# Optimization experiments

Hardware: AMD Instinct MI355X
Metric: run time of the kernel (lower is better)

Reference implementation:

```python
import jax, jax.numpy as jnp
import numpy as np

K = 10  # topk classes


def setup_inputs() -> dict:
    key = jax.random.key(0)
    ks = jax.random.split(key, 12)
    B, DF, M, C, V, DW, DT = 64, 768, 26, 3129, 10000, 300, 1024
    s = lambda k, sh, scale: jax.random.normal(k, sh, dtype=jnp.float32) * scale
    return {
        "ftm": s(ks[0], (B, DF, M, M), 1.0),
        "logits": s(ks[1], (B, C), 1.0),
        "labels": jax.random.randint(ks[2], (B,), 0, C, dtype=jnp.int32),
        "indices_table": jax.random.randint(ks[3], (C, 4), 0, V, dtype=jnp.int32),
        "word2vec": s(ks[4], (V, DW), 1.0),
        "W_emb": s(ks[5], (DW, DT), 1.0 / np.sqrt(DW)),
        "b_emb": jnp.zeros((DT,), jnp.float32),
        "W_cls": s(ks[6], (DT, DT), 1.0 / np.sqrt(DT)),
        "b_cls": jnp.zeros((DT,), jnp.float32),
        "W_v": s(ks[7], (DF, DT), 1.0 / np.sqrt(DF)),
        "b_v": jnp.zeros((DT,), jnp.float32),
        "W_bap": s(ks[8], (DT, DT), 1.0 / np.sqrt(DT)),
        "b_bap": jnp.zeros((DT,), jnp.float32),
        "W_fc": s(ks[9], (DT, K), 1.0 / np.sqrt(DT)),
        "b_fc": jnp.zeros((K,), jnp.float32),
    }


def reference(ftm, logits, labels, indices_table, word2vec,
              W_emb, b_emb, W_cls, b_cls, W_v, b_v, W_bap, b_bap, W_fc, b_fc):
    B, DF = ftm.shape[0], ftm.shape[1]
    C = logits.shape[1]
    # dispatch: topk classes, gather their word indices, embed
    _, topk_idx = jax.lax.top_k(logits, K)                  # [B, K]
    topk_cls = indices_table[topk_idx]                      # [B, K, 4]
    emb = word2vec[topk_cls].mean(axis=2)                   # [B, K, 300] (ClassEmbedding pooling)
    cls_emb = jax.nn.relu(emb @ W_emb + b_emb)              # [B, K, 1024]
    # SAC_BAP (dropouts in eval mode = identity)
    cls_emb = jax.nn.relu(cls_emb @ W_cls + b_cls)          # [B, K, 1024]
    f = ftm.reshape(B, DF, -1).transpose(0, 2, 1)           # [B, F, 768], F = m*m
    v = jax.nn.relu(f @ W_v + b_v)                          # [B, F, 1024]
    att_w_b_sfx = jnp.einsum('bfd,bkd->bfk', v, cls_emb)    # [B, F, K]
    att_w = jax.nn.softmax(att_w_b_sfx, axis=1)             # softmax over positions
    bap = jnp.einsum('bfd,bfk,bkd->bd', v, att_w, cls_emb)  # [B, 1024]
    bap = jax.nn.relu(bap @ W_bap + b_bap)                  # bap_emb_FC
    bap_logits = bap @ W_fc + b_fc                          # fc_new 1x1 conv -> [B, K]
    # combine: scatter topk logits into the full class space
    um = jnp.zeros((B, C), dtype=bap_logits.dtype)
    um = um.at[jnp.arange(B)[:, None], topk_idx].set(bap_logits)
    return um
```

## Files before the change

kernel.cpp:

```cpp
#include <hip/hip_runtime.h>
#include <hip/hip_bf16.h>

#define B_   64
#define C_   3129
#define K_   10
#define DF_  768
#define F_   676
#define DW_  300
#define DWP_ 320
#define DT_  1024
#define NSEG 13
#define FSEG 52

typedef __attribute__((ext_vector_type(8))) short short8;
typedef __attribute__((ext_vector_type(4))) float floatx4;

__device__ __forceinline__ void gload_lds16(const void* g, void* l) {
    __builtin_amdgcn_global_load_lds(
        (const __attribute__((address_space(1))) void*)g,
        (__attribute__((address_space(3))) void*)l, 16, 0, 0);
}

__global__ void topk_kernel(const float* __restrict__ logits,
                            int* __restrict__ topk_idx) {
    __shared__ float vals[C_];
    __shared__ float red_v[256];
    __shared__ int   red_i[256];
    int b = blockIdx.x;
    int tid = threadIdx.x;
    for (int i = tid; i < C_; i += 256) vals[i] = logits[(size_t)b * C_ + i];
    __syncthreads();
    for (int sel = 0; sel < K_; ++sel) {
        float bv = -INFINITY; int bi = 0x7fffffff;
        for (int i = tid; i < C_; i += 256) {
            float v = vals[i];
            if (v > bv) { bv = v; bi = i; }
        }
        red_v[tid] = bv; red_i[tid] = bi;
        __syncthreads();
        for (int s = 128; s > 0; s >>= 1) {
            if (tid < s) {
                float ov = red_v[tid + s]; int oi = red_i[tid + s];
                if (ov > red_v[tid] || (ov == red_v[tid] && oi < red_i[tid])) {
                    red_v[tid] = ov; red_i[tid] = oi;
                }
            }
            __syncthreads();
        }
        if (tid == 0) {
            topk_idx[b * K_ + sel] = red_i[0];
            vals[red_i[0]] = -INFINITY;
        }
        __syncthreads();
    }
}

__global__ void emb_kernel(const int* __restrict__ topk_idx,
                           const int* __restrict__ indices_table,
                           const float* __restrict__ word2vec,
                           __hip_bfloat16* __restrict__ emb) {
    int idx = blockIdx.x * blockDim.x + threadIdx.x;
    if (idx >= B_ * K_ * DWP_) return;
    int j  = idx % DWP_;
    int bk = idx / DWP_;
    float s = 0.f;
    if (j < DW_) {
        int cls = topk_idx[bk];
        const int* tbl = indices_table + (size_t)cls * 4;
        #pragma unroll
        for (int i = 0; i < 4; ++i) s += word2vec[(size_t)tbl[i] * DW_ + j];
        s *= 0.25f;
    }
    emb[idx] = (__hip_bfloat16)s;
}

__device__ __forceinline__ void tp_body(const float* __restrict__ s,
                                        __hip_bfloat16* __restrict__ d,
                                        int R, int Cc, int Rp, int c0, int r0) {
    __shared__ float tile[64][65];
    int t = threadIdx.x;
    int cl = (t & 15) * 4;
    int rl = t >> 4;
    #pragma unroll
    for (int i = 0; i < 4; ++i) {
        int r = rl + i * 16;
        float4 v = make_float4(0.f, 0.f, 0.f, 0.f);
        if (r0 + r < R && c0 + cl < Cc)
            v = *(const float4*)(s + (size_t)(r0 + r) * Cc + c0 + cl);
        tile[r][cl + 0] = v.x; tile[r][cl + 1] = v.y;
        tile[r][cl + 2] = v.z; tile[r][cl + 3] = v.w;
    }
    __syncthreads();
    int cw = t >> 2;
    int r4 = (t & 3) * 16;
    if (c0 + cw < Cc) {
        __align__(16) __hip_bfloat16 buf[16];
        #pragma unroll
        for (int j = 0; j < 16; ++j) buf[j] = (__hip_bfloat16)tile[r4 + j][cw];
        float4* dp = (float4*)(d + (size_t)(c0 + cw) * Rp + r0 + r4);
        dp[0] = *(float4*)&buf[0];
        dp[1] = *(float4*)&buf[8];
    }
}

__global__ __launch_bounds__(256)
void transpose_ftm(const float* __restrict__ src, __hip_bfloat16* __restrict__ dst) {
    tp_body(src + (size_t)blockIdx.z * DF_ * F_,
            dst + (size_t)blockIdx.z * F_ * DF_,
            DF_, F_, DF_, blockIdx.x * 64, blockIdx.y * 64);
}

__global__ __launch_bounds__(256)
void transpose_weights(const float* __restrict__ Wemb, __hip_bfloat16* __restrict__ WembT,
                       const float* __restrict__ Wcls, __hip_bfloat16* __restrict__ WclsT,
                       const float* __restrict__ Wv,   __hip_bfloat16* __restrict__ WvT,
                       const float* __restrict__ Wbap, __hip_bfloat16* __restrict__ WbapT) {
    int id = blockIdx.x;
    const float* s; __hip_bfloat16* d; int R, Rp;
    if (id < 80)       { s = Wemb; d = WembT; R = DW_;  Rp = DWP_; }
    else if (id < 336) { s = Wcls; d = WclsT; R = DT_;  Rp = DT_;  id -= 80;  }
    else if (id < 528) { s = Wv;   d = WvT;   R = DF_;  Rp = DF_;  id -= 336; }
    else               { s = Wbap; d = WbapT; R = DT_;  Rp = DT_;  id -= 528; }
    int bx = id & 15;
    int by = id >> 4;
    tp_body(s, d, R, DT_, Rp, bx * 64, by * 64);
}

template <int RELU, int OUTBF>
__global__ __launch_bounds__(256)
void gemm_mfma(const __hip_bfloat16* __restrict__ A,
               const __hip_bfloat16* __restrict__ Bt,
               const float* __restrict__ bias,
               void* __restrict__ Cout, int M, int N, int Kp) {
    __shared__ __align__(16) char smem[34816];
    __hip_bfloat16* As = (__hip_bfloat16*)smem;
    __hip_bfloat16* Bs = As + 128 * 64;
    int tid = threadIdx.x;
    int wave = tid >> 6, lane = tid & 63;
    int quad = lane >> 4, l16 = lane & 15;
    int wm = (wave & 1) * 64, wn = (wave >> 1) * 64;

    int gx = gridDim.x;
    int nwg = gx * gridDim.y;
    int flat = blockIdx.y * gx + blockIdx.x;
    int q = nwg >> 3, r = nwg & 7;
    int xcd = flat & 7, lid = flat >> 3;
    int o = (xcd < r ? xcd * (q + 1) : r * (q + 1) + (xcd - r) * q) + lid;
    int n0 = (o % gx) * 128;
    int m0 = (o / gx) * 128;

    floatx4 acc[4][4];
    #pragma unroll
    for (int i = 0; i < 4; ++i)
        #pragma unroll
        for (int j = 0; j < 4; ++j)
            acc[i][j] = (floatx4){0.f, 0.f, 0.f, 0.f};

    int rsub = lane >> 3;
    int gchunk = (lane & 7) ^ rsub;

    int arow[4], brow[4];
    #pragma unroll
    for (int i = 0; i < 4; ++i) {
        arow[i] = wm + i * 16 + l16;
        brow[i] = wn + i * 16 + l16;
    }

    for (int k0 = 0; k0 < Kp; k0 += 64) {
        #pragma unroll
        for (int c = 0; c < 4; ++c) {
            int grp = wave * 4 + c;
            int row = grp * 8 + rsub;
            int ra = m0 + row; if (ra >= M) ra = M - 1;
            gload_lds16(A + (size_t)ra * Kp + k0 + gchunk * 8, As + grp * 512);
            gload_lds16(Bt + (size_t)(n0 + row) * Kp + k0 + gchunk * 8, Bs + grp * 512);
        }
        __syncthreads();
        #pragma unroll
        for (int ks = 0; ks < 2; ++ks) {
            short8 af[4], bf[4];
            #pragma unroll
            for (int mi = 0; mi < 4; ++mi)
                af[mi] = *(const short8*)&As[arow[mi] * 64 +
                            ((((ks << 2) | quad) ^ (arow[mi] & 7)) << 3)];
            #pragma unroll
            for (int ni = 0; ni < 4; ++ni)
                bf[ni] = *(const short8*)&Bs[brow[ni] * 64 +
                            ((((ks << 2) | quad) ^ (brow[ni] & 7)) << 3)];
            #pragma unroll
            for (int mi = 0; mi < 4; ++mi)
                #pragma unroll
                for (int ni = 0; ni < 4; ++ni)
                    acc[mi][ni] = __builtin_amdgcn_mfma_f32_16x16x32_bf16(
                        af[mi], bf[ni], acc[mi][ni], 0, 0, 0);
        }
        __syncthreads();
    }

    float bn[4];
    #pragma unroll
    for (int ni = 0; ni < 4; ++ni) bn[ni] = bias[n0 + wn + ni * 16 + l16];

    if (OUTBF) {
        __hip_bfloat16* Cs = (__hip_bfloat16*)smem;
        #pragma unroll
        for (int mi = 0; mi < 4; ++mi)
            #pragma unroll
            for (int rr = 0; rr < 4; ++rr) {
                int row = wm + mi * 16 + quad * 4 + rr;
                #pragma unroll
                for (int ni = 0; ni < 4; ++ni) {
                    float val = acc[mi][ni][rr] + bn[ni];
                    if (RELU) val = fmaxf(val, 0.f);
                    Cs[row * 136 + wn + ni * 16 + l16] = (__hip_bfloat16)val;
                }
            }
        __syncthreads();
        #pragma unroll
        for (int j = 0; j < 8; ++j) {
            int ch = tid + 256 * j;
            int row = ch >> 4, c16 = ch & 15;
            int r = m0 + row;
            float4 val = *(const float4*)&Cs[row * 136 + c16 * 8];
            if (r < M)
                *(float4*)((__hip_bfloat16*)Cout + (size_t)r * N + n0 + c16 * 8) = val;
        }
    } else {
        #pragma unroll
        for (int mi = 0; mi < 4; ++mi)
            #pragma unroll
            for (int rr = 0; rr < 4; ++rr) {
                int r = m0 + wm + mi * 16 + quad * 4 + rr;
                if (r < M) {
                    #pragma unroll
                    for (int ni = 0; ni < 4; ++ni) {
                        float val = acc[mi][ni][rr] + bn[ni];
                        if (RELU) val = fmaxf(val, 0.f);
                        ((float*)Cout)[(size_t)r * N + n0 + wn + ni * 16 + l16] = val;
                    }
                }
            }
    }
}

__global__ __launch_bounds__(256)
void attn_s_kernel(const __hip_bfloat16* __restrict__ v_buf,
                   const __hip_bfloat16* __restrict__ cls,
                   float* __restrict__ s_buf, int b0) {
    int tid = threadIdx.x;
    int wave = tid >> 6, lane = tid & 63;
    int bc = blockIdx.y;
    int f0 = blockIdx.x * 8 + wave * 2;
    int fa = f0 < F_ ? f0 : F_ - 1;
    int fb = (f0 + 1) < F_ ? f0 + 1 : F_ - 1;
    union U { float4 f4; __hip_bfloat16 h[8]; };
    const float4* va = (const float4*)(v_buf + ((size_t)(bc * F_ + fa)) * DT_ + lane * 16);
    const float4* vb = (const float4*)(v_buf + ((size_t)(bc * F_ + fb)) * DT_ + lane * 16);
    U a0, a1, b0u, b1u;
    a0.f4 = va[0]; a1.f4 = va[1];
    b0u.f4 = vb[0]; b1u.f4 = vb[1];
    float av[16], bv[16];
    #pragma unroll
    for (int i = 0; i < 8; ++i) {
        av[i] = (float)a0.h[i]; av[8 + i] = (float)a1.h[i];
        bv[i] = (float)b0u.h[i]; bv[8 + i] = (float)b1u.h[i];
    }
    const __hip_bfloat16* cp = cls + ((size_t)(b0 + bc) * K_) * DT_ + lane * 16;
    #pragma unroll
    for (int k = 0; k < K_; ++k) {
        const float4* c4 = (const float4*)(cp + (size_t)k * DT_);
        U c0u, c1u; c0u.f4 = c4[0]; c1u.f4 = c4[1];
        float da = 0.f, db = 0.f;
        #pragma unroll
        for (int i = 0; i < 8; ++i) {
            float cl0 = (float)c0u.h[i], cl1 = (float)c1u.h[i];
            da += av[i] * cl0 + av[8 + i] * cl1;
            db += bv[i] * cl0 + bv[8 + i] * cl1;
        }
        #pragma unroll
        for (int off = 32; off > 0; off >>= 1) {
            da += __shfl_down(da, off);
            db += __shfl_down(db, off);
        }
        if (lane == 0) {
            if (f0 < F_)     s_buf[((size_t)(bc * F_) + f0) * K_ + k] = da;
            if (f0 + 1 < F_) s_buf[((size_t)(bc * F_) + f0 + 1) * K_ + k] = db;
        }
    }
}

__global__ __launch_bounds__(64)
void softmax_stats(const float* __restrict__ s_buf, float2* __restrict__ ml,
                   int b0) {
    int k = blockIdx.x, bc = blockIdx.y, lane = threadIdx.x;
    const float* sp = s_buf + (size_t)bc * F_ * K_ + k;
    float m = -INFINITY;
    for (int f = lane; f < F_; f += 64) m = fmaxf(m, sp[(size_t)f * K_]);
    #pragma unroll
    for (int off = 32; off > 0; off >>= 1) m = fmaxf(m, __shfl_xor(m, off));
    float l = 0.f;
    for (int f = lane; f < F_; f += 64) l += __expf(sp[(size_t)f * K_] - m);
    #pragma unroll
    for (int off = 32; off > 0; off >>= 1) l += __shfl_xor(l, off);
    if (lane == 0) ml[(size_t)(b0 + bc) * K_ + k] = make_float2(m, 1.f / l);
}

__global__ __launch_bounds__(256)
void o_bap_partial(const __hip_bfloat16* __restrict__ v_buf,
                   const float* __restrict__ s_buf,
                   const float2* __restrict__ ml,
                   const __hip_bfloat16* __restrict__ cls,
                   float* __restrict__ pp, int b0) {
    int bc = blockIdx.x, seg = blockIdx.y;
    int b = b0 + bc;
    int t = threadIdx.x;
    int f0 = seg * FSEG;
    __shared__ float wbuf[FSEG * K_];
    __shared__ float mk[K_], rlk[K_];
    __shared__ float red[128 * 8];
    if (t < K_) {
        float2 v = ml[(size_t)b * K_ + t];
        mk[t] = v.x; rlk[t] = v.y;
    }
    __syncthreads();
    for (int j = t; j < FSEG * K_; j += 256) {
        int k = j % K_;
        float sv = s_buf[((size_t)bc * F_ + f0) * K_ + j];
        wbuf[j] = __expf(sv - mk[k]) * rlk[k];
    }
    __syncthreads();
    int th = t & 127, half = t >> 7;
    int d0 = th * 8;
    int fs = half * (FSEG / 2);
    float acc[K_][8] = {};
    const __hip_bfloat16* vp = v_buf + ((size_t)bc * F_ + f0 + fs) * DT_ + d0;
    for (int f = 0; f < FSEG / 2; ++f) {
        union { float4 f4; __hip_bfloat16 h[8]; } u;
        u.f4 = *(const float4*)(vp + (size_t)f * DT_);
        float vv[8];
        #pragma unroll
        for (int i = 0; i < 8; ++i) vv[i] = (float)u.h[i];
        const float* wk = &wbuf[(fs + f) * K_];
        #pragma unroll
        for (int k = 0; k < K_; ++k)
            #pragma unroll
            for (int i = 0; i < 8; ++i) acc[k][i] += wk[k] * vv[i];
    }
    float outv[8] = {};
    union { float4 f4; __hip_bfloat16 h[8]; } cu;
    #pragma unroll
    for (int k = 0; k < K_; ++k) {
        cu.f4 = *(const float4*)(cls + ((size_t)b * K_ + k) * DT_ + d0);
        #pragma unroll
        for (int i = 0; i < 8; ++i) outv[i] += acc[k][i] * (float)cu.h[i];
    }
    if (half == 1) {
        *(float4*)&red[th * 8]     = *(float4*)&outv[0];
        *(float4*)&red[th * 8 + 4] = *(float4*)&outv[4];
    }
    __syncthreads();
    if (half == 0) {
        #pragma unroll
        for (int i = 0; i < 8; ++i) outv[i] += red[th * 8 + i];
        float* pd = pp + ((size_t)seg * B_ + b) * DT_ + d0;
        *(float4*)pd       = *(float4*)&outv[0];
        *(float4*)(pd + 4) = *(float4*)&outv[4];
    }
}

__global__ void bap_combine(const float* __restrict__ pp,
                            __hip_bfloat16* __restrict__ bap) {
    int idx = blockIdx.x * 256 + threadIdx.x;
    float s = 0.f;
    #pragma unroll
    for (int g = 0; g < NSEG; ++g) s += pp[idx + (size_t)g * B_ * DT_];
    bap[idx] = (__hip_bfloat16)s;
}

__global__ void final_kernel(const float* __restrict__ y,
                             const float* __restrict__ Wfc,
                             const float* __restrict__ bfc,
                             const int* __restrict__ topk_idx,
                             float* __restrict__ out) {
    int b = blockIdx.x, tid = threadIdx.x;
    int lane = tid & 63, wave = tid >> 6;
    float pk[K_] = {};
    for (int d = tid; d < DT_; d += 256) {
        float yv = y[(size_t)b * DT_ + d];
        #pragma unroll
        for (int k = 0; k < K_; ++k) pk[k] += yv * Wfc[(size_t)d * K_ + k];
    }
    __shared__ float wsum[4][K_];
    #pragma unroll
    for (int k = 0; k < K_; ++k) {
        float a = pk[k];
        #pragma unroll
        for (int off = 32; off > 0; off >>= 1) a += __shfl_down(a, off);
        if (lane == 0) wsum[wave][k] = a;
    }
    __syncthreads();
    if (tid < K_) {
        float lg = wsum[0][tid] + wsum[1][tid] + wsum[2][tid] + wsum[3][tid] + bfc[tid];
        out[(size_t)b * C_ + topk_idx[b * K_ + tid]] = lg;
    }
}

extern "C" void kernel_launch(void* const* d_in, const int* in_sizes, int n_in,
                              void* d_out, int out_size, void* d_ws, size_t ws_size,
                              hipStream_t stream) {
    const float* ftm           = (const float*)d_in[0];
    const float* logits        = (const float*)d_in[1];
    const int*   indices_table = (const int*)d_in[3];
    const float* word2vec      = (const float*)d_in[4];
    const float* W_emb         = (const float*)d_in[5];
    const float* b_emb         = (const float*)d_in[6];
    const float* W_cls         = (const float*)d_in[7];
    const float* b_cls         = (const float*)d_in[8];
    const float* W_v           = (const float*)d_in[9];
    const float* b_v           = (const float*)d_in[10];
    const float* W_bap         = (const float*)d_in[11];
    const float* b_bap         = (const float*)d_in[12];
    const float* W_fc          = (const float*)d_in[13];
    const float* b_fc          = (const float*)d_in[14];
    float* out = (float*)d_out;

    char* ws = (char*)d_ws;
    size_t off = 0;
    auto alloc = [&](size_t bytes) -> void* {
        void* p = ws + off;
        off = (off + bytes + 255) & ~(size_t)255;
        return p;
    };
    int*            topk_idx = (int*)           alloc((size_t)B_ * K_ * 4);
    __hip_bfloat16* emb_bf   = (__hip_bfloat16*)alloc((size_t)B_ * K_ * DWP_ * 2);
    __hip_bfloat16* cls1     = (__hip_bfloat16*)alloc((size_t)B_ * K_ * DT_ * 2);
    __hip_bfloat16* cls2     = (__hip_bfloat16*)alloc((size_t)B_ * K_ * DT_ * 2);
    __hip_bfloat16* Wemb_t   = (__hip_bfloat16*)alloc((size_t)DT_ * DWP_ * 2);
    __hip_bfloat16* Wcls_t   = (__hip_bfloat16*)alloc((size_t)DT_ * DT_ * 2);
    __hip_bfloat16* Wv_t     = (__hip_bfloat16*)alloc((size_t)DT_ * DF_ * 2);
    __hip_bfloat16* Wbap_t   = (__hip_bfloat16*)alloc((size_t)DT_ * DT_ * 2);
    float*          s_buf    = (float*)         alloc((size_t)B_ * F_ * K_ * 4);
    float2*         ml       = (float2*)        alloc((size_t)B_ * K_ * 8);
    float*          pp       = (float*)         alloc((size_t)NSEG * B_ * DT_ * 4);
    __hip_bfloat16* bap_bf   = (__hip_bfloat16*)alloc((size_t)B_ * DT_ * 2);
    float*          yb       = (float*)         alloc((size_t)B_ * DT_ * 4);

    size_t per_b = (size_t)F_ * DF_ * 2 + (size_t)F_ * DT_ * 2;
    size_t avail = (ws_size > off + 8192) ? ws_size - off - 8192 : 0;
    int nb = (int)(avail / per_b);
    if (nb > B_) nb = B_;
    if (nb < 1) nb = 1;
    __hip_bfloat16* ftm_t = (__hip_bfloat16*)alloc((size_t)nb * F_ * DF_ * 2);
    __hip_bfloat16* v_buf = (__hip_bfloat16*)alloc((size_t)nb * F_ * DT_ * 2);

    hipMemsetAsync(d_out, 0, (size_t)out_size * sizeof(float), stream);

    topk_kernel<<<B_, 256, 0, stream>>>(logits, topk_idx);
    emb_kernel<<<(B_ * K_ * DWP_ + 255) / 256, 256, 0, stream>>>(
        topk_idx, indices_table, word2vec, emb_bf);

    transpose_weights<<<784, 256, 0, stream>>>(
        W_emb, Wemb_t, W_cls, Wcls_t, W_v, Wv_t, W_bap, Wbap_t);

    gemm_mfma<1, 1><<<dim3(DT_ / 128, (B_ * K_ + 127) / 128), 256, 0, stream>>>(
        emb_bf, Wemb_t, b_emb, cls1, B_ * K_, DT_, DWP_);
    gemm_mfma<1, 1><<<dim3(DT_ / 128, (B_ * K_ + 127) / 128), 256, 0, stream>>>(
        cls1, Wcls_t, b_cls, cls2, B_ * K_, DT_, DT_);

    for (int b0 = 0; b0 < B_; b0 += nb) {
        int cb = min(nb, B_ - b0);
        transpose_ftm<<<dim3((F_ + 63) / 64, DF_ / 64, cb), 256, 0, stream>>>(
            ftm + (size_t)b0 * DF_ * F_, ftm_t);
        int M = cb * F_;
        gemm_mfma<1, 1><<<dim3(DT_ / 128, (M + 127) / 128), 256, 0, stream>>>(
            ftm_t, Wv_t, b_v, v_buf, M, DT_, DF_);
        float* s_c = s_buf + (size_t)b0 * F_ * K_;
        attn_s_kernel<<<dim3((F_ + 7) / 8, cb), 256, 0, stream>>>(
            v_buf, cls2, s_c, b0);
        softmax_stats<<<dim3(K_, cb), 64, 0, stream>>>(s_c, ml, b0);
        o_bap_partial<<<dim3(cb, NSEG), 256, 0, stream>>>(
            v_buf, s_c, ml, cls2, pp, b0);
    }
    bap_combine<<<B_ * DT_ / 256, 256, 0, stream>>>(pp, bap_bf);

    gemm_mfma<1, 0><<<dim3(DT_ / 128, 1), 256, 0, stream>>>(
        bap_bf, Wbap_t, b_bap, yb, B_, DT_, DT_);
    final_kernel<<<B_, 256, 0, stream>>>(yb, W_fc, b_fc, topk_idx, out);
}
```

Measured before the change: 479.7 us.

## Add 256x256 MFMA GEMM with XCD-aware block remap for the visual projection

```diff
diff --git a/kernel.cpp b/kernel.cpp
--- a/kernel.cpp
+++ b/kernel.cpp
@@ -240,6 +240,149 @@
                     }
                 }
             }
+    }
+}
+
+__global__ __launch_bounds__(512, 2)
+void gemm_mfma256(const __hip_bfloat16* __restrict__ A,
+                  const __hip_bfloat16* __restrict__ Bt,
+                  const float* __restrict__ bias,
+                  __hip_bfloat16* __restrict__ Cout, int M, int N, int Kp) {
+    __shared__ __align__(16) __hip_bfloat16 smem[65536];
+    int tid = threadIdx.x;
+    int wave = tid >> 6, lane = tid & 63;
+    int quad = lane >> 4, l16 = lane & 15;
+    int wr = wave >> 2, wc = wave & 3;
+
+    int gx = gridDim.x;
+    int nwg = gx * gridDim.y;
+    int flat = blockIdx.y * gx + blockIdx.x;
+    int q = nwg >> 3, r = nwg & 7;
+    int xcd = flat & 7, lid = flat >> 3;
+    int o = (xcd < r ? xcd * (q + 1) : r * (q + 1) + (xcd - r) * q) + lid;
+    int n0 = (o % gx) * 256;
+    int m0 = (o / gx) * 256;
+
+    floatx4 acc[8][4];
+    #pragma unroll
+    for (int i = 0; i < 8; ++i)
+        #pragma unroll
+        for (int j = 0; j < 4; ++j)
+            acc[i][j] = (floatx4){0.f, 0.f, 0.f, 0.f};
+
+    int rsub = lane >> 3;
+    int gchunk = (lane & 7) ^ rsub;
+
+    int rowA[8], rowB[4], kchunk[2];
+    #pragma unroll
+    for (int i = 0; i < 8; ++i) rowA[i] = (wr * 128 + i * 16 + l16) * 64;
+    #pragma unroll
+    for (int i = 0; i < 4; ++i) rowB[i] = (wc * 64 + i * 16 + l16) * 64;
+    #pragma unroll
+    for (int ks = 0; ks < 2; ++ks)
+        kchunk[ks] = ((((ks << 2) | quad) ^ (l16 & 7)) << 3);
+
+    const int NT = Kp >> 6;
+
+    {
+        __hip_bfloat16* Ad = smem;
+        __hip_bfloat16* Bd = smem + 16384;
+        #pragma unroll
+        for (int c = 0; c < 4; ++c) {
+            int g = wave * 4 + c;
+            int row = g * 8 + rsub;
+            gload_lds16(A + (size_t)(m0 + row) * Kp + gchunk * 8, Ad + g * 512);
+            gload_lds16(Bt + (size_t)(n0 + row) * Kp + gchunk * 8, Bd + g * 512);
+        }
+    }
+
+    for (int kt = 0; kt < NT; ++kt) {
+        int cur = kt & 1;
+        if (kt + 1 < NT) {
+            __hip_bfloat16* Ad = smem + (cur ^ 1) * 32768;
+            __hip_bfloat16* Bd = Ad + 16384;
+            int k0n = (kt + 1) << 6;
+            #pragma unroll
+            for (int c = 0; c < 4; ++c) {
+                int g = wave * 4 + c;
+                int row = g * 8 + rsub;
+                gload_lds16(A + (size_t)(m0 + row) * Kp + k0n + gchunk * 8,
+                            Ad + g * 512);
+                gload_lds16(Bt + (size_t)(n0 + row) * Kp + k0n + gchunk * 8,
+                            Bd + g * 512);
+            }
+            asm volatile("s_waitcnt vmcnt(8)" ::: "memory");
+        } else {
+            asm volatile("s_waitcnt vmcnt(0)" ::: "memory");
+        }
+        __builtin_amdgcn_s_barrier();
+
+        const __hip_bfloat16* As = smem + cur * 32768;
+        const __hip_bfloat16* Bs = As + 16384;
+
+        short8 af[4][2], bf2[2][2];
+        #pragma unroll
+        for (int ph = 0; ph < 4; ++ph) {
+            const int h = ph >> 1, j = ph & 1;
+            if (j == 0) {
+                #pragma unroll
+                for (int mi = 0; mi < 4; ++mi)
+                    #pragma unroll
+                    for (int ks = 0; ks < 2; ++ks)
+                        af[mi][ks] = *(const short8*)&As[rowA[h * 4 + mi] + kchunk[ks]];
+            }
+            #pragma unroll
+            for (int ni = 0; ni < 2; ++ni)
+                #pragma unroll
+                for (int ks = 0; ks < 2; ++ks)
+                    bf2[ni][ks] = *(const short8*)&Bs[rowB[j * 2 + ni] + kchunk[ks]];
+            __builtin_amdgcn_s_barrier();
+            __builtin_amdgcn_s_setprio(1);
+            #pragma unroll
+            for (int ks = 0; ks < 2; ++ks)
+                #pragma unroll
+                for (int mi = 0; mi < 4; ++mi)
+                    #pragma unroll
+                    for (int ni = 0; ni < 2; ++ni)
+                        acc[h * 4 + mi][j * 2 + ni] =
+                            __builtin_amdgcn_mfma_f32_16x16x32_bf16(
+                                af[mi][ks], bf2[ni][ks],
+                                acc[h * 4 + mi][j * 2 + ni], 0, 0, 0);
+            __builtin_amdgcn_s_setprio(0);
+            __builtin_amdgcn_s_barrier();
+        }
+    }
+
+    float bn[4];
+    #pragma unroll
+    for (int ni = 0; ni < 4; ++ni) bn[ni] = bias[n0 + wc * 64 + ni * 16 + l16];
+
+    __hip_bfloat16* Cs = smem;
+    #pragma unroll
+    for (int half = 0; half < 2; ++half) {
+        if (wr == half) {
+            #pragma unroll
+            for (int mi = 0; mi < 8; ++mi)
+                #pragma unroll
+                for (int rr = 0; rr < 4; ++rr) {
+                    int row = mi * 16 + quad * 4 + rr;
+                    #pragma unroll
+                    for (int ni = 0; ni < 4; ++ni) {
+                        float val = acc[mi][ni][rr] + bn[ni];
+                        val = fmaxf(val, 0.f);
+                        Cs[row * 264 + wc * 64 + ni * 16 + l16] = (__hip_bfloat16)val;
+                    }
+                }
+        }
+        __syncthreads();
+        #pragma unroll
+        for (int s = 0; s < 8; ++s) {
+            int ch = tid + 512 * s;
+            int row = ch >> 5, c32 = ch & 31;
+            float4 val = *(const float4*)&Cs[row * 264 + c32 * 8];
+            *(float4*)(Cout + (size_t)(m0 + half * 128 + row) * N + n0 + c32 * 8) = val;
+        }
+        __syncthreads();
     }
 }
 
@@ -472,8 +615,13 @@
         transpose_ftm<<<dim3((F_ + 63) / 64, DF_ / 64, cb), 256, 0, stream>>>(
             ftm + (size_t)b0 * DF_ * F_, ftm_t);
         int M = cb * F_;
-        gemm_mfma<1, 1><<<dim3(DT_ / 128, (M + 127) / 128), 256, 0, stream>>>(
-            ftm_t, Wv_t, b_v, v_buf, M, DT_, DF_);
+        if ((M & 255) == 0) {
+            gemm_mfma256<<<dim3(DT_ / 256, M / 256), 512, 0, stream>>>(
+                ftm_t, Wv_t, b_v, v_buf, M, DT_, DF_);
+        } else {
+            gemm_mfma<1, 1><<<dim3(DT_ / 128, (M + 127) / 128), 256, 0, stream>>>(
+                ftm_t, Wv_t, b_v, v_buf, M, DT_, DF_);
+        }
         float* s_c = s_buf + (size_t)b0 * F_ * K_;
         attn_s_kernel<<<dim3((F_ + 7) / 8, cb), 256, 0, stream>>>(
             v_buf, cls2, s_c, b0);
```

New measurement: 487.0 us. About the same (+1.5%).
